# Optimization experiments

Hardware: AMD Instinct MI355X
Metric: run time of the kernel (lower is better)

## Reference

```python
import jax, jax.numpy as jnp
import numpy as np

B, S, D, H = 4, 2048, 1024, 16
HD = D // H

def setup_inputs() -> dict:
    key = jax.random.key(0)
    ks = jax.random.split(key, 11)
    s = 1.0 / np.sqrt(D)
    return {
        "q": jax.random.normal(ks[0], (B, S, D), jnp.float32),
        "k": jax.random.normal(ks[1], (B, S, D), jnp.float32),
        "v": jax.random.normal(ks[2], (B, S, D), jnp.float32),
        "Wq": jax.random.normal(ks[3], (D, D), jnp.float32) * s,
        "bq": jax.random.normal(ks[4], (D,), jnp.float32) * 0.01,
        "Wk": jax.random.normal(ks[5], (D, D), jnp.float32) * s,
        "bk": jax.random.normal(ks[6], (D,), jnp.float32) * 0.01,
        "Wv": jax.random.normal(ks[7], (D, D), jnp.float32) * s,
        "bv": jax.random.normal(ks[8], (D,), jnp.float32) * 0.01,
        "Wo": jax.random.normal(ks[9], (D, D), jnp.float32) * s,
        "bo": jax.random.normal(ks[10], (D,), jnp.float32) * 0.01,
    }

def reference(q, k, v, Wq, bq, Wk, bk, Wv, bv, Wo, bo):
    # linear projections + ReLU activation (as in the torch module)
    qh = jax.nn.relu(q @ Wq.T + bq)
    kh = jax.nn.relu(k @ Wk.T + bk)
    vh = jax.nn.relu(v @ Wv.T + bv)
    # split heads: [B,S,D] -> [B,H,S,HD]
    def split(x):
        return x.reshape(B, S, H, HD).transpose(0, 2, 1, 3)
    qh, kh, vh = split(qh), split(kh), split(vh)
    scale = 1.0 / np.sqrt(HD).astype(np.float32)
    scores = jnp.einsum("bhqd,bhkd->bhqk", qh, kh) * scale
    attn = jax.nn.softmax(scores, axis=-1)
    y = jnp.einsum("bhqk,bhkd->bhqd", attn, vh)
    # merge heads: [B,H,S,HD] -> [B,S,D]
    y = y.transpose(0, 2, 1, 3).reshape(B, S, D)
    return jax.nn.relu(y @ Wo.T + bo)
```

## Files before the change

### kernel.cpp

```cpp
#include <hip/hip_runtime.h>
#include <hip/hip_bf16.h>
#include <cstdint>
#include <cstddef>

#define Bc 4
#define Sc 2048
#define Dc 1024
#define Hc 16

typedef __bf16 bf16;
typedef bf16  bf16x4 __attribute__((ext_vector_type(4)));
typedef bf16  bf16x8 __attribute__((ext_vector_type(8)));
typedef float f32x4  __attribute__((ext_vector_type(4)));

__device__ __forceinline__ void load_lds16(const bf16* g, bf16* l) {
    __builtin_amdgcn_global_load_lds((const __attribute__((address_space(1))) void*)g,
                                     (__attribute__((address_space(3))) void*)l,
                                     16, 0, 0);
}

__device__ __forceinline__ void cvt16(const float* __restrict__ g,
                                      bf16x8& lo, bf16x8& hi) {
    const f32x4 a0 = *(const f32x4*)(g);
    const f32x4 a1 = *(const f32x4*)(g + 4);
    const f32x4 a2 = *(const f32x4*)(g + 8);
    const f32x4 a3 = *(const f32x4*)(g + 12);
#pragma unroll
    for (int j = 0; j < 4; j++) {
        lo[j]     = (bf16)a0[j];
        lo[j + 4] = (bf16)a1[j];
        hi[j]     = (bf16)a2[j];
        hi[j + 4] = (bf16)a3[j];
    }
}

__device__ __forceinline__ void store_relu(float* p, float v) { *p = fmaxf(v, 0.0f); }
__device__ __forceinline__ void store_relu(bf16*  p, float v) { *p = (bf16)fmaxf(v, 0.0f); }

__global__ __launch_bounds__(256)
void cvt_f32_bf16(const float* __restrict__ src, bf16* __restrict__ dst, int n16) {
    const int idx = blockIdx.x * 256 + threadIdx.x;
    if (idx >= n16) return;
    bf16x8 lo, hi;
    cvt16(src + (size_t)idx * 16, lo, hi);
    *(bf16x8*)(dst + (size_t)idx * 16)     = lo;
    *(bf16x8*)(dst + (size_t)idx * 16 + 8) = hi;
}

#define BM 128
#define BN 128
#define BK 64

template <typename TC, bool TR>
__global__ __launch_bounds__(256)
void gemm_bb(const bf16* __restrict__ A, const bf16* __restrict__ W,
             const float* __restrict__ bias, TC* __restrict__ C,
             int M, int N, int K) {
    constexpr int POOL = TR ? 36864 : 32768;
    __shared__ __align__(16) char pool[POOL];
    bf16* lA = (bf16*)pool;
    bf16* lB = (bf16*)(pool + 16384);

    const int t    = threadIdx.x;
    const int lane = t & 63;
    const int wave = t >> 6;
    const int l15  = lane & 15;
    const int quad = lane >> 4;

    const int m0 = blockIdx.x * BM;
    const int n0 = blockIdx.y * BN;
    const int wm = (wave >> 1) * 64;
    const int wn = (wave & 1) * 64;

    f32x4 acc[4][4] = {};

    const int srow = t >> 3;
    const int cg   = (((t & 7) ^ (srow & 7)) << 3);
    const bf16* gA = A + (size_t)(m0 + srow) * K + cg;
    const bf16* gW = W + (size_t)(n0 + srow) * K + cg;
    bf16* lA0 = lA + t * 8;
    bf16* lB0 = lB + t * 8;

    for (int k0 = 0; k0 < K; k0 += BK) {
        __syncthreads();
#pragma unroll
        for (int c = 0; c < 4; c++) {
            load_lds16(gA + (size_t)(32 * c) * K, lA0 + c * 2048);
            load_lds16(gW + (size_t)(32 * c) * K, lB0 + c * 2048);
        }
        gA += BK; gW += BK;
        __syncthreads();

#pragma unroll
        for (int ks = 0; ks < 2; ks++) {
            bf16x8 af[4], bfr[4];
#pragma unroll
            for (int mt = 0; mt < 4; mt++) {
                const int row = wm + mt * 16 + l15;
                const int colp = ((((ks << 2) | quad) ^ (l15 & 7)) << 3);
                af[mt] = *(const bf16x8*)(lA + row * BK + colp);
            }
#pragma unroll
            for (int nt = 0; nt < 4; nt++) {
                const int row = wn + nt * 16 + l15;
                const int colp = ((((ks << 2) | quad) ^ (l15 & 7)) << 3);
                bfr[nt] = *(const bf16x8*)(lB + row * BK + colp);
            }
#pragma unroll
            for (int mt = 0; mt < 4; mt++)
#pragma unroll
                for (int nt = 0; nt < 4; nt++)
                    acc[mt][nt] = __builtin_amdgcn_mfma_f32_16x16x32_bf16(
                        af[mt], bfr[nt], acc[mt][nt], 0, 0, 0);
        }
    }

    if constexpr (!TR) {
#pragma unroll
        for (int nt = 0; nt < 4; nt++) {
            const int col = n0 + wn + nt * 16 + l15;
            const float bv = bias[col];
#pragma unroll
            for (int mt = 0; mt < 4; mt++) {
                const int rowb = m0 + wm + mt * 16 + quad * 4;
#pragma unroll
                for (int i = 0; i < 4; i++)
                    store_relu(&C[(size_t)(rowb + i) * N + col], acc[mt][nt][i] + bv);
            }
        }
    } else {
        __syncthreads();
        bf16* trp = (bf16*)pool;
#pragma unroll
        for (int nt = 0; nt < 4; nt++) {
            const int col = n0 + wn + nt * 16 + l15;
            const float bv = bias[col];
#pragma unroll
            for (int mt = 0; mt < 4; mt++)
#pragma unroll
                for (int i = 0; i < 4; i++)
                    trp[((wave * 64) + nt * 16 + l15) * 72 + mt * 16 + quad * 4 + i] =
                        (bf16)fmaxf(acc[mt][nt][i] + bv, 0.0f);
        }
        __syncthreads();
        const int r2 = lane >> 3;
        const int c8 = (lane & 7) * 8;
#pragma unroll
        for (int rr = 0; rr < 8; rr++) {
            const int rt = rr * 8 + r2;
            const bf16x8 vv = *(const bf16x8*)&trp[((wave * 64) + rt) * 72 + c8];
            const int cg2 = n0 + wn + rt;
            const int h   = cg2 >> 6, hd = cg2 & 63;
            const int mg  = m0 + wm + c8;
            const int b   = mg >> 11, s = mg & (Sc - 1);
            bf16* dst = (bf16*)C + ((size_t)(b * Hc + h) * 64 + hd) * Sc + s;
            *(bf16x8*)dst = vv;
        }
    }
}

#define QI 4

__global__ __launch_bounds__(256)
void attn_flash(const bf16* __restrict__ Qh, const bf16* __restrict__ Kh,
                const bf16* __restrict__ Vt_g, bf16* __restrict__ Y) {
    __shared__ __align__(16) bf16 Kl[64][72];
    __shared__ __align__(16) bf16 Vl[64][72];
    __shared__ __align__(16) bf16 Pl[4][64][72];

    const int t    = threadIdx.x;
    const int lane = t & 63;
    const int wave = t >> 6;
    const int l15  = lane & 15;
    const int quad = lane >> 4;

    const int qt = blockIdx.x;
    const int bh = blockIdx.y;
    const int b  = bh >> 4;
    const int h  = bh & 15;
    const int q0 = qt * 256;
    const size_t rowbase = (size_t)b * Sc;
    const size_t vhead   = (size_t)(b * Hc + h) * 64;

    const float qscale = 0.125f * 1.44269504f;
    bf16x8 qf[QI][2];
#pragma unroll
    for (int qi = 0; qi < QI; qi++) {
        const bf16* qp = Qh + (rowbase + q0 + wave * 64 + qi * 16 + l15) * (size_t)Dc + h * 64;
#pragma unroll
        for (int ks = 0; ks < 2; ks++) {
            const bf16x8 raw = *(const bf16x8*)(qp + ks * 32 + quad * 8);
#pragma unroll
            for (int j = 0; j < 8; j++) qf[qi][ks][j] = (bf16)((float)raw[j] * qscale);
        }
    }

    bf16x8 ones;
#pragma unroll
    for (int j = 0; j < 8; j++) ones[j] = (bf16)1.0f;

    f32x4 yacc[QI][4] = {};
    f32x4 sacc[QI]    = {};

    const int sr = t >> 2;
    const int sc = (t & 3) * 16;
    constexpr int NT = Sc / 64;

    const bf16* kp = Kh + (rowbase + sr) * (size_t)Dc + h * 64 + sc;
    const bf16* vp = Vt_g + (vhead + sr) * (size_t)Sc + sc;
    bf16x8 k0 = *(const bf16x8*)kp;
    bf16x8 k1 = *(const bf16x8*)(kp + 8);
    bf16x8 v0 = *(const bf16x8*)vp;
    bf16x8 v1 = *(const bf16x8*)(vp + 8);

    for (int kt = 0; kt < NT; kt++) {
        __syncthreads();
        *(bf16x8*)&Kl[sr][sc]     = k0;
        *(bf16x8*)&Kl[sr][sc + 8] = k1;
        *(bf16x8*)&Vl[sr][sc]     = v0;
        *(bf16x8*)&Vl[sr][sc + 8] = v1;
        __syncthreads();

        if (kt + 1 < NT) {
            kp += (size_t)64 * Dc;
            vp += 64;
            k0 = *(const bf16x8*)kp;
            k1 = *(const bf16x8*)(kp + 8);
            v0 = *(const bf16x8*)vp;
            v1 = *(const bf16x8*)(vp + 8);
        }

        bf16x8 kf[4][2];
#pragma unroll
        for (int mt = 0; mt < 4; mt++) {
            kf[mt][0] = *(const bf16x8*)&Kl[mt * 16 + l15][quad * 8];
            kf[mt][1] = *(const bf16x8*)&Kl[mt * 16 + l15][32 + quad * 8];
        }

#pragma unroll
        for (int qi = 0; qi < QI; qi++) {
            f32x4 s[4];
            __builtin_amdgcn_s_setprio(1);
#pragma unroll
            for (int mt = 0; mt < 4; mt++) {
                s[mt] = (f32x4){0.f, 0.f, 0.f, 0.f};
                s[mt] = __builtin_amdgcn_mfma_f32_16x16x32_bf16(
                    kf[mt][0], qf[qi][0], s[mt], 0, 0, 0);
                s[mt] = __builtin_amdgcn_mfma_f32_16x16x32_bf16(
                    kf[mt][1], qf[qi][1], s[mt], 0, 0, 0);
            }
            __builtin_amdgcn_s_setprio(0);
#pragma unroll
            for (int mt = 0; mt < 4; mt++) {
                bf16x4 pk;
#pragma unroll
                for (int i = 0; i < 4; i++)
                    pk[i] = (bf16)__builtin_amdgcn_exp2f(s[mt][i]);
                *(bf16x4*)&Pl[wave][qi * 16 + l15][mt * 16 + quad * 4] = pk;
            }
        }

        bf16x8 vf[4][2];
#pragma unroll
        for (int nt = 0; nt < 4; nt++) {
            vf[nt][0] = *(const bf16x8*)&Vl[nt * 16 + l15][quad * 8];
            vf[nt][1] = *(const bf16x8*)&Vl[nt * 16 + l15][32 + quad * 8];
        }

        bf16x8 pf[QI][2];
#pragma unroll
        for (int qi = 0; qi < QI; qi++) {
            pf[qi][0] = *(const bf16x8*)&Pl[wave][qi * 16 + l15][quad * 8];
            pf[qi][1] = *(const bf16x8*)&Pl[wave][qi * 16 + l15][32 + quad * 8];
        }
        __builtin_amdgcn_s_setprio(1);
#pragma unroll
        for (int qi = 0; qi < QI; qi++) {
            sacc[qi] = __builtin_amdgcn_mfma_f32_16x16x32_bf16(ones, pf[qi][0], sacc[qi], 0, 0, 0);
            sacc[qi] = __builtin_amdgcn_mfma_f32_16x16x32_bf16(ones, pf[qi][1], sacc[qi], 0, 0, 0);
#pragma unroll
            for (int nt = 0; nt < 4; nt++) {
                yacc[qi][nt] = __builtin_amdgcn_mfma_f32_16x16x32_bf16(
                    vf[nt][0], pf[qi][0], yacc[qi][nt], 0, 0, 0);
                yacc[qi][nt] = __builtin_amdgcn_mfma_f32_16x16x32_bf16(
                    vf[nt][1], pf[qi][1], yacc[qi][nt], 0, 0, 0);
            }
        }
        __builtin_amdgcn_s_setprio(0);
    }

#pragma unroll
    for (int qi = 0; qi < QI; qi++) {
        const float inv = 1.0f / sacc[qi][0];
        bf16* yp = Y + (rowbase + q0 + wave * 64 + qi * 16 + l15) * (size_t)Dc + h * 64;
#pragma unroll
        for (int nt = 0; nt < 4; nt++)
#pragma unroll
            for (int i = 0; i < 4; i++)
                yp[nt * 16 + quad * 4 + i] = (bf16)(yacc[qi][nt][i] * inv);
    }
}

extern "C" void kernel_launch(void* const* d_in, const int* in_sizes, int n_in,
                              void* d_out, int out_size, void* d_ws, size_t ws_size,
                              hipStream_t stream) {
    const float* q  = (const float*)d_in[0];
    const float* k  = (const float*)d_in[1];
    const float* v  = (const float*)d_in[2];
    const float* Wq = (const float*)d_in[3];
    const float* bq = (const float*)d_in[4];
    const float* Wk = (const float*)d_in[5];
    const float* bk = (const float*)d_in[6];
    const float* Wv = (const float*)d_in[7];
    const float* bv = (const float*)d_in[8];
    const float* Wo = (const float*)d_in[9];
    const float* bo = (const float*)d_in[10];
    float* out = (float*)d_out;

    const int M = Bc * Sc;
    const int N = Dc;
    const int K = Dc;
    const size_t E  = (size_t)Bc * Sc * Dc;
    const size_t EW = (size_t)Dc * Dc;

    bf16* Qh   = (bf16*)d_out;
    bf16* Kh   = Qh + E;
    bf16* tmpA = (bf16*)d_ws;
    bf16* VtG  = tmpA + E;
    bf16* Wqb  = VtG + E;
    bf16* Wkb  = Wqb + EW;
    bf16* Wvb  = Wkb + EW;
    bf16* Wob  = Wvb + EW;

    const int n16  = (int)(E / 16);
    const int n16w = (int)(EW / 16);
    dim3 gc(n16 / 256);
    dim3 gw(n16w / 256);
    dim3 gg(M / BM, N / BN);
    dim3 ga(Sc / 256, Bc * Hc);

    cvt_f32_bf16<<<gw, 256, 0, stream>>>(Wq, Wqb, n16w);
    cvt_f32_bf16<<<gw, 256, 0, stream>>>(Wk, Wkb, n16w);
    cvt_f32_bf16<<<gw, 256, 0, stream>>>(Wv, Wvb, n16w);
    cvt_f32_bf16<<<gw, 256, 0, stream>>>(Wo, Wob, n16w);

    cvt_f32_bf16<<<gc, 256, 0, stream>>>(q, tmpA, n16);
    gemm_bb<bf16, false><<<gg, 256, 0, stream>>>(tmpA, Wqb, bq, Qh, M, N, K);

    cvt_f32_bf16<<<gc, 256, 0, stream>>>(k, tmpA, n16);
    gemm_bb<bf16, false><<<gg, 256, 0, stream>>>(tmpA, Wkb, bk, Kh, M, N, K);

    cvt_f32_bf16<<<gc, 256, 0, stream>>>(v, tmpA, n16);
    gemm_bb<bf16, true><<<gg, 256, 0, stream>>>(tmpA, Wvb, bv, VtG, M, N, K);

    attn_flash<<<ga, 256, 0, stream>>>(Qh, Kh, VtG, tmpA);

    gemm_bb<float, false><<<gg, 256, 0, stream>>>(tmpA, Wob, bo, out, M, N, K);
}
```

Before: 379.7 us.

## Double-buffer attention K/V tiles, shrink P scratch, batch weight conversions

The attention loop now double-buffers the K/V shared-memory tiles and drops one of its two barriers per iteration. It also loads V fragments early and processes query sub-tiles in pairs, so the per-wave P scratch shrinks from 64 rows to 32, cutting LDS use and possibly raising occupancy. Separately, the four weight conversion launches are merged into one 2D-grid kernel to cut launch overhead. The cost is more registers live at once (the V fragments), which could hurt occupancy.

```diff
diff --git a/kernel.cpp b/kernel.cpp
--- a/kernel.cpp
+++ b/kernel.cpp
@@ -45,6 +45,20 @@
     cvt16(src + (size_t)idx * 16, lo, hi);
     *(bf16x8*)(dst + (size_t)idx * 16)     = lo;
     *(bf16x8*)(dst + (size_t)idx * 16 + 8) = hi;
+}
+
+__global__ __launch_bounds__(256)
+void cvt_w4(const float* __restrict__ s0, const float* __restrict__ s1,
+            const float* __restrict__ s2, const float* __restrict__ s3,
+            bf16* __restrict__ dst) {
+    const float* srcs[4] = {s0, s1, s2, s3};
+    const float* src = srcs[blockIdx.y];
+    const int idx = blockIdx.x * 256 + threadIdx.x;
+    bf16x8 lo, hi;
+    cvt16(src + (size_t)idx * 16, lo, hi);
+    bf16* d = dst + (size_t)blockIdx.y * ((size_t)Dc * Dc) + (size_t)idx * 16;
+    *(bf16x8*)d       = lo;
+    *(bf16x8*)(d + 8) = hi;
 }
 
 #define BM 128
@@ -164,9 +178,9 @@
 __global__ __launch_bounds__(256)
 void attn_flash(const bf16* __restrict__ Qh, const bf16* __restrict__ Kh,
                 const bf16* __restrict__ Vt_g, bf16* __restrict__ Y) {
-    __shared__ __align__(16) bf16 Kl[64][72];
-    __shared__ __align__(16) bf16 Vl[64][72];
-    __shared__ __align__(16) bf16 Pl[4][64][72];
+    __shared__ __align__(16) bf16 Kl[2][64][72];
+    __shared__ __align__(16) bf16 Vl[2][64][72];
+    __shared__ __align__(16) bf16 Pl[4][2][16][72];
 
     const int t    = threadIdx.x;
     const int lane = t & 63;
@@ -214,12 +228,11 @@
     bf16x8 v1 = *(const bf16x8*)(vp + 8);
 
     for (int kt = 0; kt < NT; kt++) {
-        __syncthreads();
-        *(bf16x8*)&Kl[sr][sc]     = k0;
-        *(bf16x8*)&Kl[sr][sc + 8] = k1;
-        *(bf16x8*)&Vl[sr][sc]     = v0;
-        *(bf16x8*)&Vl[sr][sc + 8] = v1;
-        __syncthreads();
+        const int cur = kt & 1;
+        *(bf16x8*)&Kl[cur][sr][sc]     = k0;
+        *(bf16x8*)&Kl[cur][sr][sc + 8] = k1;
+        *(bf16x8*)&Vl[cur][sr][sc]     = v0;
+        *(bf16x8*)&Vl[cur][sr][sc + 8] = v1;
 
         if (kt + 1 < NT) {
             kp += (size_t)64 * Dc;
@@ -230,63 +243,68 @@
             v1 = *(const bf16x8*)(vp + 8);
         }
 
-        bf16x8 kf[4][2];
+        __syncthreads();
+
+        bf16x8 kf[4][2], vf[4][2];
 #pragma unroll
         for (int mt = 0; mt < 4; mt++) {
-            kf[mt][0] = *(const bf16x8*)&Kl[mt * 16 + l15][quad * 8];
-            kf[mt][1] = *(const bf16x8*)&Kl[mt * 16 + l15][32 + quad * 8];
-        }
-
-#pragma unroll
-        for (int qi = 0; qi < QI; qi++) {
-            f32x4 s[4];
+            kf[mt][0] = *(const bf16x8*)&Kl[cur][mt * 16 + l15][quad * 8];
+            kf[mt][1] = *(const bf16x8*)&Kl[cur][mt * 16 + l15][32 + quad * 8];
+        }
+#pragma unroll
+        for (int nt = 0; nt < 4; nt++) {
+            vf[nt][0] = *(const bf16x8*)&Vl[cur][nt * 16 + l15][quad * 8];
+            vf[nt][1] = *(const bf16x8*)&Vl[cur][nt * 16 + l15][32 + quad * 8];
+        }
+
+#pragma unroll
+        for (int qp = 0; qp < 2; qp++) {
+#pragma unroll
+            for (int qq = 0; qq < 2; qq++) {
+                const int qi = qp * 2 + qq;
+                f32x4 s[4];
+                __builtin_amdgcn_s_setprio(1);
+#pragma unroll
+                for (int mt = 0; mt < 4; mt++) {
+                    s[mt] = (f32x4){0.f, 0.f, 0.f, 0.f};
+                    s[mt] = __builtin_amdgcn_mfma_f32_16x16x32_bf16(
+                        kf[mt][0], qf[qi][0], s[mt], 0, 0, 0);
+                    s[mt] = __builtin_amdgcn_mfma_f32_16x16x32_bf16(
+                        kf[mt][1], qf[qi][1], s[mt], 0, 0, 0);
+                }
+                __builtin_amdgcn_s_setprio(0);
+#pragma unroll
+                for (int mt = 0; mt < 4; mt++) {
+                    bf16x4 pk;
+#pragma unroll
+                    for (int i = 0; i < 4; i++)
+                        pk[i] = (bf16)__builtin_amdgcn_exp2f(s[mt][i]);
+                    *(bf16x4*)&Pl[wave][qq][l15][mt * 16 + quad * 4] = pk;
+                }
+            }
+
+            bf16x8 pf[2][2];
+#pragma unroll
+            for (int qq = 0; qq < 2; qq++) {
+                pf[qq][0] = *(const bf16x8*)&Pl[wave][qq][l15][quad * 8];
+                pf[qq][1] = *(const bf16x8*)&Pl[wave][qq][l15][32 + quad * 8];
+            }
             __builtin_amdgcn_s_setprio(1);
 #pragma unroll
-            for (int mt = 0; mt < 4; mt++) {
-                s[mt] = (f32x4){0.f, 0.f, 0.f, 0.f};
-                s[mt] = __builtin_amdgcn_mfma_f32_16x16x32_bf16(
-                    kf[mt][0], qf[qi][0], s[mt], 0, 0, 0);
-                s[mt] = __builtin_amdgcn_mfma_f32_16x16x32_bf16(
-                    kf[mt][1], qf[qi][1], s[mt], 0, 0, 0);
+            for (int qq = 0; qq < 2; qq++) {
+                const int qi = qp * 2 + qq;
+                sacc[qi] = __builtin_amdgcn_mfma_f32_16x16x32_bf16(ones, pf[qq][0], sacc[qi], 0, 0, 0);
+                sacc[qi] = __builtin_amdgcn_mfma_f32_16x16x32_bf16(ones, pf[qq][1], sacc[qi], 0, 0, 0);
+#pragma unroll
+                for (int nt = 0; nt < 4; nt++) {
+                    yacc[qi][nt] = __builtin_amdgcn_mfma_f32_16x16x32_bf16(
+                        vf[nt][0], pf[qq][0], yacc[qi][nt], 0, 0, 0);
+                    yacc[qi][nt] = __builtin_amdgcn_mfma_f32_16x16x32_bf16(
+                        vf[nt][1], pf[qq][1], yacc[qi][nt], 0, 0, 0);
+                }
             }
             __builtin_amdgcn_s_setprio(0);
-#pragma unroll
-            for (int mt = 0; mt < 4; mt++) {
-                bf16x4 pk;
-#pragma unroll
-                for (int i = 0; i < 4; i++)
-                    pk[i] = (bf16)__builtin_amdgcn_exp2f(s[mt][i]);
-                *(bf16x4*)&Pl[wave][qi * 16 + l15][mt * 16 + quad * 4] = pk;
-            }
-        }
-
-        bf16x8 vf[4][2];
-#pragma unroll
-        for (int nt = 0; nt < 4; nt++) {
-            vf[nt][0] = *(const bf16x8*)&Vl[nt * 16 + l15][quad * 8];
-            vf[nt][1] = *(const bf16x8*)&Vl[nt * 16 + l15][32 + quad * 8];
-        }
-
-        bf16x8 pf[QI][2];
-#pragma unroll
-        for (int qi = 0; qi < QI; qi++) {
-            pf[qi][0] = *(const bf16x8*)&Pl[wave][qi * 16 + l15][quad * 8];
-            pf[qi][1] = *(const bf16x8*)&Pl[wave][qi * 16 + l15][32 + quad * 8];
-        }
-        __builtin_amdgcn_s_setprio(1);
-#pragma unroll
-        for (int qi = 0; qi < QI; qi++) {
-            sacc[qi] = __builtin_amdgcn_mfma_f32_16x16x32_bf16(ones, pf[qi][0], sacc[qi], 0, 0, 0);
-            sacc[qi] = __builtin_amdgcn_mfma_f32_16x16x32_bf16(ones, pf[qi][1], sacc[qi], 0, 0, 0);
-#pragma unroll
-            for (int nt = 0; nt < 4; nt++) {
-                yacc[qi][nt] = __builtin_amdgcn_mfma_f32_16x16x32_bf16(
-                    vf[nt][0], pf[qi][0], yacc[qi][nt], 0, 0, 0);
-                yacc[qi][nt] = __builtin_amdgcn_mfma_f32_16x16x32_bf16(
-                    vf[nt][1], pf[qi][1], yacc[qi][nt], 0, 0, 0);
-            }
-        }
-        __builtin_amdgcn_s_setprio(0);
+        }
     }
 
 #pragma unroll
@@ -335,14 +353,11 @@
     const int n16  = (int)(E / 16);
     const int n16w = (int)(EW / 16);
     dim3 gc(n16 / 256);
-    dim3 gw(n16w / 256);
+    dim3 gw4(n16w / 256, 4);
     dim3 gg(M / BM, N / BN);
     dim3 ga(Sc / 256, Bc * Hc);
 
-    cvt_f32_bf16<<<gw, 256, 0, stream>>>(Wq, Wqb, n16w);
-    cvt_f32_bf16<<<gw, 256, 0, stream>>>(Wk, Wkb, n16w);
-    cvt_f32_bf16<<<gw, 256, 0, stream>>>(Wv, Wvb, n16w);
-    cvt_f32_bf16<<<gw, 256, 0, stream>>>(Wo, Wob, n16w);
+    cvt_w4<<<gw4, 256, 0, stream>>>(Wq, Wk, Wv, Wo, Wqb);
 
     cvt_f32_bf16<<<gc, 256, 0, stream>>>(q, tmpA, n16);
     gemm_bb<bf16, false><<<gg, 256, 0, stream>>>(tmpA, Wqb, bq, Qh, M, N, K);
```

New measurement: 382.2 us. No clear change (+0.7%).
